# Optimization experiments

Hardware: AMD Instinct MI355X
Metric: run time of the kernel (lower is better)

## Reference

```python
import jax, jax.numpy as jnp
import numpy as np
from jax import lax

V, T, L = 32, 8192, 16
JITTER = 1e-6
LOG2PI = float(np.log(2.0 * np.pi))


def _state_space(lengthscale, variance):
    # Matern-3/2 SDE state space: lam = sqrt(3)/ell, P0 = diag(var, var*lam^2)
    lam = jnp.sqrt(3.0) / lengthscale                      # [L]
    z = jnp.zeros_like(lam)
    P0 = jnp.stack([jnp.stack([variance, z], -1),
                    jnp.stack([z, variance * lam ** 2], -1)], -2)  # [L,2,2]
    return lam, P0


def _state_transition(dt, lam):
    # dt: [v,T,1,1,1]; lam: [L] -> A = expm(F*dt): [v,L,T,2,2]
    lam3 = lam[:, None, None]                              # [L,1,1]
    ldt = dt * lam3                                        # [v,T,L,1,1]
    e = jnp.exp(-ldt)
    a11 = e * (ldt + 1.0)
    a12 = e * jnp.broadcast_to(dt, ldt.shape)
    a21 = -e * lam3 * ldt
    a22 = e * (1.0 - ldt)
    A = jnp.concatenate([jnp.concatenate([a11, a12], -1),
                         jnp.concatenate([a21, a22], -1)], -2)  # [v,T,L,2,2]
    return jnp.swapaxes(A, 1, 2)                           # [v,L,T,2,2]


def _mT(x):
    return jnp.swapaxes(x, -1, -2)


def _update_posterior(dt_nonzero, pseudo_y, pseudo_var, lengthscale, variance):
    v, Tn, Ln = pseudo_y.shape
    dtype = pseudo_y.dtype
    lam, P0 = _state_space(lengthscale, variance)
    P0b4 = P0[:, None]                                     # [L,1,2,2]
    zeros = jnp.zeros((v, 1, 1, 1, 1), dtype)

    # ---------------- filter (dt starts with 0) ----------------
    dt_f = jnp.concatenate([zeros, dt_nonzero], axis=1)    # [v,T,1,1,1]
    A_f = _state_transition(dt_f, lam)                     # [v,L,T,2,2]
    Q_f = P0b4 - A_f @ P0b4 @ _mT(A_f)
    A_t = jnp.moveaxis(A_f, 2, 0)                          # [T,v,L,2,2]
    Q_t = jnp.moveaxis(Q_f, 2, 0)
    ys = jnp.transpose(pseudo_y, (1, 0, 2))                # [T,v,L]
    rs = jnp.transpose(pseudo_var, (1, 0, 2))
    H = jnp.array([[1.0, 0.0]], dtype=dtype)               # [1,2]

    m0 = jnp.zeros((v, Ln, 2, 1), dtype)
    P0c = jnp.broadcast_to(P0, (v, Ln, 2, 2))

    def filt_step(carry, x):
        m, P = carry
        A, Q, y, r = x                                     # A/Q: [v,L,2,2]; y/r: [v,L]
        m_p = A @ m                                        # [v,L,2,1]
        P_p = A @ P @ _mT(A) + Q                           # [v,L,2,2]
        hat = (H @ m_p)[..., 0, 0]                         # [v,L]
        HP = H @ P_p                                       # [v,L,1,2]
        s = (HP @ H.T)[..., 0, 0] + r                      # [v,L] innovation var (1x1)
        d = y - hat                                        # [v,L]
        log_p = -0.5 * (d * d / s + jnp.log(s) + LOG2PI)   # MVN(1-dim) log prob
        W = _mT(HP) / (s + JITTER)[..., None, None]        # [v,L,2,1] Kalman gain
        m_new = m_p + W * d[..., None, None]
        P_new = P_p - W @ HP
        return (m_new, P_new), (m_new, P_new, log_p)

    (_, _), (m_fs_t, P_fs_t, log_ps) = lax.scan(filt_step, (m0, P0c), (A_t, Q_t, ys, rs))
    sum_log_p = jnp.sum(log_ps, axis=(0, 2))               # sum over T then L -> [v]
    m_fs = jnp.moveaxis(m_fs_t, 0, 2)                      # [v,L,T,2,1]
    P_fs = jnp.moveaxis(P_fs_t, 0, 2)                      # [v,L,T,2,2]

    # ---------------- RTS smoother (dt ends with 0) ----------------
    dt_s = jnp.concatenate([dt_nonzero, zeros], axis=1)
    A_s = _state_transition(dt_s, lam)
    Q_s = P0b4 - A_s @ P0b4 @ _mT(A_s)
    xs = (m_fs_t, P_fs_t, jnp.moveaxis(A_s, 2, 0), jnp.moveaxis(Q_s, 2, 0))
    I2 = jnp.eye(2, dtype=dtype)

    def smooth_step(carry, x):
        m_s, P_s = carry
        m_f, P_f, A, Q = x
        m_p = A @ m_f
        A_Pf = A @ P_f
        P_p = A_Pf @ _mT(A) + Q
        G = _mT(jnp.linalg.solve(P_p + JITTER * I2, A_Pf))  # [v,L,2,2]
        m_s2 = m_f + G @ (m_s - m_p)
        P_s2 = P_f - G @ (P_s - P_p) @ _mT(G)
        mZ = (H @ m_s2)[..., 0, 0]                          # [v,L]
        PZ = (H @ P_s2 @ H.T)[..., 0, 0]                    # [v,L]
        return (m_s2, P_s2), (mZ, PZ)

    carry0 = (m_fs[:, :, -1], P_fs[:, :, -1])
    (_, _), (mZ_t, PZ_t) = lax.scan(smooth_step, carry0, xs, reverse=True)
    m_ss_Z = jnp.transpose(mZ_t, (1, 2, 0))                 # [v,L,T]
    P_ss_Z = jnp.transpose(PZ_t, (1, 2, 0))                 # [v,L,T]
    return m_fs, P_fs, m_ss_Z, P_ss_Z, sum_log_p


def setup_inputs() -> dict:
    key = jax.random.key(0)
    k1, k2, k3, k4, k5 = jax.random.split(key, 5)
    dt_nonzero = jax.random.uniform(k1, (V, T - 1, 1, 1, 1), jnp.float32) * 0.05 + 0.01
    pseudo_y = jax.random.normal(k2, (V, T, L), jnp.float32)
    pseudo_var = jax.random.uniform(k3, (V, T, L), jnp.float32) * 0.5 + 0.1
    lengthscale = jax.random.uniform(k4, (L,), jnp.float32) + 1.0
    variance = jax.random.uniform(k5, (L,), jnp.float32) * 0.5 + 0.5
    return {"dt_nonzero": dt_nonzero, "pseudo_y": pseudo_y, "pseudo_var": pseudo_var,
            "lengthscale": lengthscale, "variance": variance}


def reference(dt_nonzero, pseudo_y, pseudo_var, lengthscale, variance):
    return _update_posterior(dt_nonzero, pseudo_y, pseudo_var, lengthscale, variance)
```

## Files before the change

### kernel.cpp

```cpp
#include <hip/hip_runtime.h>

#define TV 32
#define TT 8192
#define TL 16
#define NCHAIN (TV * TL)
#define CHUNK 32
#define WARM 96
#define NCHUNK (TT / CHUNK)
#define JIT 1e-6f
#define C_LOG2PI 1.837877066409345483560659472811f

#define BF 16

__global__ void __launch_bounds__(256)
__attribute__((amdgpu_waves_per_eu(2, 2)))
kf_fwd(
    const float* __restrict__ dt,
    const float* __restrict__ y,
    const float* __restrict__ rvar,
    const float* __restrict__ ls,
    const float* __restrict__ var,
    float* __restrict__ m_fs,
    float* __restrict__ P_fs,
    float* __restrict__ slp)
{
    const int tid   = blockIdx.x * 256 + threadIdx.x;
    const int chain = tid & (NCHAIN - 1);
    const int chunk = tid / NCHAIN;
    const int v = chain >> 4;
    const int l = chain & 15;

    const float lam = 1.7320508075688772f / ls[l];
    const float v0  = var[l];
    const float v1  = v0 * lam * lam;

    const int s  = chunk * CHUNK;
    const int e  = s + CHUNK;
    const int u0 = (s >= WARM) ? (s - WARM) : 0;

    const float* dtv = dt + (size_t)v * (TT - 1);
    const float* yp  = y    + (size_t)v * TT * TL + l;
    const float* rp  = rvar + (size_t)v * TT * TL + l;
    float4* mo4 = (float4*)(m_fs + (size_t)chain * TT * 2);
    float4* Po  = (float4*)(P_fs + (size_t)chain * TT * 4);

    float m0 = 0.f, m1 = 0.f;
    float P00 = v0, P01 = 0.f, P11 = v1;
    float acc = 0.f;
    float bm0 = 0.f, bm1 = 0.f;

    float ya[BF], ra[BF], da[BF];
    float yb[BF], rb[BF], db[BF];

#define FLOAD(Y, R, D, tb) {                                                  \
    _Pragma("unroll")                                                         \
    for (int j = 0; j < BF; ++j) {                                            \
        const int tt_ = (tb) + j;                                             \
        Y[j] = yp[(size_t)tt_ * TL];                                          \
        R[j] = rp[(size_t)tt_ * TL];                                          \
        D[j] = dtv[(tt_ >= 1) ? (tt_ - 1) : 0];                               \
    }                                                                         \
}

#define FCOMP(Y, R, D, tb) {                                                  \
    _Pragma("unroll")                                                         \
    for (int j = 0; j < BF; ++j) {                                            \
        const int tt_ = (tb) + j;                                             \
        const float dtc = (tt_ == 0) ? 0.f : D[j];  \
        const float ldt = dtc * lam;                                          \
        const float ee  = __expf(-ldt);                                       \
        const float a11 = ee * (ldt + 1.f);                                   \
        const float a12 = ee * dtc;                                           \
        const float a21 = -ee * lam * ldt;                                    \
        const float a22 = ee * (1.f - ldt);                                   \
        const float q00 = v0 - (a11 * a11 * v0 + a12 * a12 * v1);             \
        const float q01 = -(a11 * a21 * v0 + a12 * a22 * v1);                 \
        const float q11 = v1 - (a21 * a21 * v0 + a22 * a22 * v1);             \
        const float mp0 = a11 * m0 + a12 * m1;                                \
        const float mp1 = a21 * m0 + a22 * m1;                                \
        const float ap00 = a11 * P00 + a12 * P01;                             \
        const float ap01 = a11 * P01 + a12 * P11;                             \
        const float ap10 = a21 * P00 + a22 * P01;                             \
        const float ap11 = a21 * P01 + a22 * P11;                             \
        const float pp00 = ap00 * a11 + ap01 * a12 + q00;                     \
        const float pp01 = ap00 * a21 + ap01 * a22 + q01;                     \
        const float pp11 = ap10 * a21 + ap11 * a22 + q11;                     \
        const float ssv  = pp00 + R[j];                                       \
        const float d    = Y[j] - mp0;                                        \
        const float sinv = __builtin_amdgcn_rcpf(ssv + JIT);                  \
        const float W0 = pp00 * sinv;                                         \
        const float W1 = pp01 * sinv;                                         \
        m0 = mp0 + W0 * d;                                                    \
        m1 = mp1 + W1 * d;                                                    \
        P00 = pp00 - W0 * pp00;                                               \
        P01 = pp01 - W0 * pp01;                                               \
        P11 = pp11 - W1 * pp01;                                               \
        if (tt_ >= s) {            \
            acc += -0.5f * (d * d * __builtin_amdgcn_rcpf(ssv)                \
                            + __logf(ssv) + C_LOG2PI);                        \
            if ((j & 1) == 0) { bm0 = m0; bm1 = m1; }            \
            else mo4[tt_ >> 1] = make_float4(bm0, bm1, m0, m1);               \
            Po[tt_] = make_float4(P00, P01, P01, P11);                        \
        }                                                                     \
    }                                                                         \
}

    FLOAD(ya, ra, da, u0);
    for (int t = u0; t < e; t += 2 * BF) {
        FLOAD(yb, rb, db, t + BF);
        FCOMP(ya, ra, da, t);
        if (t + 2 * BF < e) FLOAD(ya, ra, da, t + 2 * BF);
        FCOMP(yb, rb, db, t + BF);
    }

    for (int mask = 8; mask >= 1; mask >>= 1)
        acc += __shfl_xor(acc, mask, 16);
    if ((threadIdx.x & 15) == 0)
        atomicAdd(&slp[v], acc);
}

#define BB 8

__global__ void __launch_bounds__(256)
__attribute__((amdgpu_waves_per_eu(2, 2)))
kf_bwd(
    const float* __restrict__ dt,
    const float* __restrict__ ls,
    const float* __restrict__ var,
    const float* __restrict__ m_fs,
    const float* __restrict__ P_fs,
    float* __restrict__ mZ,
    float* __restrict__ PZ)
{
    const int tid   = blockIdx.x * 256 + threadIdx.x;
    const int chain = tid & (NCHAIN - 1);
    const int chunk = tid / NCHAIN;
    const int v = chain >> 4;
    const int l = chain & 15;

    const float lam = 1.7320508075688772f / ls[l];
    const float v0  = var[l];
    const float v1  = v0 * lam * lam;

    const int s = chunk * CHUNK;
    const int e = s + CHUNK;
    int t0 = e - 1 + WARM;
    if (t0 > TT - 1) t0 = TT - 1;

    const float* dtv = dt + (size_t)v * (TT - 1);
    const float2* mi  = (const float2*)(m_fs + (size_t)chain * TT * 2);
    const float4* mi4 = (const float4*)(m_fs + (size_t)chain * TT * 2);
    const float4* Pi  = (const float4*)(P_fs + (size_t)chain * TT * 4);
    float* mo = mZ + (size_t)chain * TT;
    float* Po = PZ + (size_t)chain * TT;

    float2 mf2 = mi[t0];
    float4 Pf4 = Pi[t0];
    float ms0 = mf2.x, ms1 = mf2.y;
    float Ps00 = Pf4.x, Ps01 = Pf4.y, Ps11 = Pf4.w;
    if (t0 < e) { mo[t0] = ms0; Po[t0] = Ps00; }

    auto step = [&](float dtc, float mf0, float mf1,
                    float Pf00, float Pf01, float Pf11) {
        const float ldt = dtc * lam;
        const float ee  = __expf(-ldt);
        const float a11 = ee * (ldt + 1.f);
        const float a12 = ee * dtc;
        const float a21 = -ee * lam * ldt;
        const float a22 = ee * (1.f - ldt);
        const float q00 = v0 - (a11 * a11 * v0 + a12 * a12 * v1);
        const float q01 = -(a11 * a21 * v0 + a12 * a22 * v1);
        const float q11 = v1 - (a21 * a21 * v0 + a22 * a22 * v1);

        const float mp0 = a11 * mf0 + a12 * mf1;
        const float mp1 = a21 * mf0 + a22 * mf1;
        const float ap00 = a11 * Pf00 + a12 * Pf01;
        const float ap01 = a11 * Pf01 + a12 * Pf11;
        const float ap10 = a21 * Pf00 + a22 * Pf01;
        const float ap11 = a21 * Pf01 + a22 * Pf11;
        const float pp00 = ap00 * a11 + ap01 * a12 + q00;
        const float pp01 = ap00 * a21 + ap01 * a22 + q01;
        const float pp11 = ap10 * a21 + ap11 * a22 + q11;

        const float M00 = pp00 + JIT, M11 = pp11 + JIT;
        const float dinv = __builtin_amdgcn_rcpf(M00 * M11 - pp01 * pp01);
        const float G00 = (M11 * ap00 - pp01 * ap10) * dinv;
        const float G01 = (-pp01 * ap00 + M00 * ap10) * dinv;
        const float G10 = (M11 * ap01 - pp01 * ap11) * dinv;
        const float G11 = (-pp01 * ap01 + M00 * ap11) * dinv;

        const float dm0 = ms0 - mp0, dm1 = ms1 - mp1;
        const float nms0 = mf0 + G00 * dm0 + G01 * dm1;
        const float nms1 = mf1 + G10 * dm0 + G11 * dm1;
        const float D00 = Ps00 - pp00, D01 = Ps01 - pp01, D11 = Ps11 - pp11;
        const float gd00 = G00 * D00 + G01 * D01;
        const float gd01 = G00 * D01 + G01 * D11;
        const float gd10 = G10 * D00 + G11 * D01;
        const float gd11 = G10 * D01 + G11 * D11;
        ms0 = nms0; ms1 = nms1;
        Ps00 = Pf00 - (gd00 * G00 + gd01 * G01);
        Ps01 = Pf01 - (gd00 * G10 + gd01 * G11);
        Ps11 = Pf11 - (gd10 * G10 + gd11 * G11);
    };

    int t = t0 - 1;
    for (; t >= s && (t & 7) != 7; --t) {
        mf2 = mi[t]; Pf4 = Pi[t];
        step(dtv[t], mf2.x, mf2.y, Pf4.x, Pf4.y, Pf4.w);
        if (t < e) { mo[t] = ms0; Po[t] = Ps00; }
    }

    float b0m = 0.f, b1m = 0.f, b2m = 0.f, b3m = 0.f;
    float b0P = 0.f, b1P = 0.f, b2P = 0.f, b3P = 0.f;

    float4 Ma[BB / 2], Pa[BB]; float Da[BB];
    float4 Mb[BB / 2], Pb[BB]; float Db[BB];

#define BLOAD(M, P, D, tb) {                                                  \
    const int ib_ = ((tb) - 7) >> 1;                                          \
    _Pragma("unroll")                                                         \
    for (int j = 0; j < BB / 2; ++j) M[j] = mi4[ib_ + j];                     \
    _Pragma("unroll")                                                         \
    for (int j = 0; j < BB; ++j) {                                            \
        const int tt_ = (tb) - j;                                             \
        P[j] = Pi[tt_];                                                       \
        D[j] = dtv[tt_];                                                      \
    }                                                                         \
}

#define BCOMP(M, P, D, tb) {                                                  \
    const bool wr_ = (tb) < e;        \
    _Pragma("unroll")                                                         \
    for (int jj = 0; jj < BB; ++jj) {                                         \
        const int tt_ = (tb) - jj;                                            \
        const int k_  = 7 - jj;             \
        const float mf0_ = (k_ & 1) ? M[k_ >> 1].z : M[k_ >> 1].x;            \
        const float mf1_ = (k_ & 1) ? M[k_ >> 1].w : M[k_ >> 1].y;            \
        step(D[jj], mf0_, mf1_, P[jj].x, P[jj].y, P[jj].w);                   \
        const int slot_ = k_ & 3;               \
        if (slot_ == 3)      { b3m = ms0; b3P = Ps00; }                       \
        else if (slot_ == 2) { b2m = ms0; b2P = Ps00; }                       \
        else if (slot_ == 1) { b1m = ms0; b1P = Ps00; }                       \
        else {                                                                \
            b0m = ms0; b0P = Ps00;                                            \
            if (wr_) {                         \
                *(float4*)(mo + tt_) = make_float4(b0m, b1m, b2m, b3m);       \
                *(float4*)(Po + tt_) = make_float4(b0P, b1P, b2P, b3P);       \
            }                                                                 \
        }                                                                     \
    }                                                                         \
}

    int nb = (t - s + 1) >> 3;
    if (nb > 0) {
        BLOAD(Ma, Pa, Da, t);
        for (; nb >= 2; nb -= 2) {
            BLOAD(Mb, Pb, Db, t - BB);
            BCOMP(Ma, Pa, Da, t);
            t -= BB;
            if (nb > 2) BLOAD(Ma, Pa, Da, t - BB);
            BCOMP(Mb, Pb, Db, t);
            t -= BB;
        }
        if (nb == 1) BCOMP(Ma, Pa, Da, t);
    }
}

extern "C" void kernel_launch(void* const* d_in, const int* in_sizes, int n_in,
                              void* d_out, int out_size, void* d_ws, size_t ws_size,
                              hipStream_t stream) {
    const float* dt  = (const float*)d_in[0];
    const float* y   = (const float*)d_in[1];
    const float* rv  = (const float*)d_in[2];
    const float* ls  = (const float*)d_in[3];
    const float* var = (const float*)d_in[4];

    float* out  = (float*)d_out;
    float* m_fs = out;
    float* P_fs = m_fs + (size_t)NCHAIN * TT * 2;
    float* mZ   = P_fs + (size_t)NCHAIN * TT * 4;
    float* PZ   = mZ + (size_t)NCHAIN * TT;
    float* slp  = PZ + (size_t)NCHAIN * TT;

    hipMemsetAsync(slp, 0, TV * sizeof(float), stream);

    const int ntask = NCHAIN * NCHUNK;
    kf_fwd<<<ntask / 256, 256, 0, stream>>>(dt, y, rv, ls, var, m_fs, P_fs, slp);
    kf_bwd<<<ntask / 256, 256, 0, stream>>>(dt, ls, var, m_fs, P_fs, mZ, PZ);
}
```

Baseline: 330.0 us.

## Replace smoother warm-up with exact chunk affine-map composition and serial scan

The forward kernel now also composes, per chunk, the affine RTS smoother map (gain product, offset, covariance term) and writes it to workspace. A new small kernel scans these chunk maps backward across the sequence to give each chunk its exact starting smoothed state. The backward kernel then starts at the chunk end with no 96-step warm-up. This removes redundant warm-up work in the backward pass but adds per-step map composition in the forward pass and a serial scan kernel over 256 chunks with only 2 blocks. Scheduling barriers were also added around the prefetch loads.

```diff
diff --git a/kernel.cpp b/kernel.cpp
--- a/kernel.cpp
+++ b/kernel.cpp
@@ -9,8 +9,9 @@
 #define NCHUNK (TT / CHUNK)
 #define JIT 1e-6f
 #define C_LOG2PI 1.837877066409345483560659472811f
-
 #define BF 16
+#define BB 8
+#define SB 8
 
 __global__ void __launch_bounds__(256)
 __attribute__((amdgpu_waves_per_eu(2, 2)))
@@ -22,7 +23,10 @@
     const float* __restrict__ var,
     float* __restrict__ m_fs,
     float* __restrict__ P_fs,
-    float* __restrict__ slp)
+    float* __restrict__ slp,
+    float4* __restrict__ g4w,
+    float2* __restrict__ b2w,
+    float4* __restrict__ e4w)
 {
     const int tid   = blockIdx.x * 256 + threadIdx.x;
     const int chain = tid & (NCHAIN - 1);
@@ -48,6 +52,10 @@
     float P00 = v0, P01 = 0.f, P11 = v1;
     float acc = 0.f;
     float bm0 = 0.f, bm1 = 0.f;
+
+    float gam00 = 1.f, gam01 = 0.f, gam10 = 0.f, gam11 = 1.f;
+    float mbc0 = 0.f, mbc1 = 0.f;
+    float me00 = 0.f, me01 = 0.f, me11 = 0.f;
 
     float ya[BF], ra[BF], da[BF];
     float yb[BF], rb[BF], db[BF];
@@ -61,6 +69,41 @@
         D[j] = dtv[(tt_ >= 1) ? (tt_ - 1) : 0];                               \
     }                                                                         \
 }
+
+#define MAPCOMPOSE(SGNPLUS)                                                   \
+    {                                                                         \
+        const float M00_ = pp00 + JIT, M11_ = pp11 + JIT;                     \
+        const float dinv_ = __builtin_amdgcn_rcpf(M00_ * M11_ - pp01 * pp01); \
+        const float g00 = (M11_ * ap00 - pp01 * ap10) * dinv_;                \
+        const float g01 = (-pp01 * ap00 + M00_ * ap10) * dinv_;               \
+        const float g10 = (M11_ * ap01 - pp01 * ap11) * dinv_;                \
+        const float g11 = (-pp01 * ap01 + M00_ * ap11) * dinv_;               \
+        const float bb0 = m0 - (g00 * mp0 + g01 * mp1);                       \
+        const float bb1 = m1 - (g10 * mp0 + g11 * mp1);                       \
+        const float gp00 = g00 * pp00 + g01 * pp01;                           \
+        const float gp01 = g00 * pp01 + g01 * pp11;                           \
+        const float gp10 = g10 * pp00 + g11 * pp01;                           \
+        const float gp11 = g10 * pp01 + g11 * pp11;                           \
+        const float ee00 = P00 + (gp00 * g00 + gp01 * g01);                   \
+        const float ee01 = P01 + (gp00 * g10 + gp01 * g11);                   \
+        const float ee11 = P11 + (gp10 * g10 + gp11 * g11);                   \
+        mbc0 += gam00 * bb0 + gam01 * bb1;                                    \
+        mbc1 += gam10 * bb0 + gam11 * bb1;                                    \
+        const float u00 = gam00 * ee00 + gam01 * ee01;                        \
+        const float u01 = gam00 * ee01 + gam01 * ee11;                        \
+        const float u10 = gam10 * ee00 + gam11 * ee01;                        \
+        const float u11 = gam10 * ee01 + gam11 * ee11;                        \
+        const float r00 = u00 * gam00 + u01 * gam01;                          \
+        const float r01 = u00 * gam10 + u01 * gam11;                          \
+        const float r11 = u10 * gam10 + u11 * gam11;                          \
+        if (SGNPLUS) { me00 += r00; me01 += r01; me11 += r11; }               \
+        else         { me00 -= r00; me01 -= r01; me11 -= r11; }               \
+        const float ng00 = gam00 * g00 + gam01 * g10;                         \
+        const float ng01 = gam00 * g01 + gam01 * g11;                         \
+        const float ng10 = gam10 * g00 + gam11 * g10;                         \
+        const float ng11 = gam10 * g01 + gam11 * g11;                         \
+        gam00 = ng00; gam01 = ng01; gam10 = ng10; gam11 = ng11;               \
+    }
 
 #define FCOMP(Y, R, D, tb) {                                                  \
     _Pragma("unroll")                                                         \
@@ -85,6 +128,7 @@
         const float pp00 = ap00 * a11 + ap01 * a12 + q00;                     \
         const float pp01 = ap00 * a21 + ap01 * a22 + q01;                     \
         const float pp11 = ap10 * a21 + ap11 * a22 + q11;                     \
+        if (tt_ > s) MAPCOMPOSE((j & 1) != 0);            \
         const float ssv  = pp00 + R[j];                                       \
         const float d    = Y[j] - mp0;                                        \
         const float sinv = __builtin_amdgcn_rcpf(ssv + JIT);                  \
@@ -106,11 +150,45 @@
 }
 
     FLOAD(ya, ra, da, u0);
+    __builtin_amdgcn_sched_barrier(0);
     for (int t = u0; t < e; t += 2 * BF) {
         FLOAD(yb, rb, db, t + BF);
+        __builtin_amdgcn_sched_barrier(0);
         FCOMP(ya, ra, da, t);
-        if (t + 2 * BF < e) FLOAD(ya, ra, da, t + 2 * BF);
+        if (t + 2 * BF < e) {
+            FLOAD(ya, ra, da, t + 2 * BF);
+            __builtin_amdgcn_sched_barrier(0);
+        }
         FCOMP(yb, rb, db, t + BF);
+    }
+
+    if (chunk != NCHUNK - 1) {
+        const float dtc = dtv[e - 1];
+        const float ldt = dtc * lam;
+        const float ee  = __expf(-ldt);
+        const float a11 = ee * (ldt + 1.f);
+        const float a12 = ee * dtc;
+        const float a21 = -ee * lam * ldt;
+        const float a22 = ee * (1.f - ldt);
+        const float q00 = v0 - (a11 * a11 * v0 + a12 * a12 * v1);
+        const float q01 = -(a11 * a21 * v0 + a12 * a22 * v1);
+        const float q11 = v1 - (a21 * a21 * v0 + a22 * a22 * v1);
+        const float mp0 = a11 * m0 + a12 * m1;
+        const float mp1 = a21 * m0 + a22 * m1;
+        const float ap00 = a11 * P00 + a12 * P01;
+        const float ap01 = a11 * P01 + a12 * P11;
+        const float ap10 = a21 * P00 + a22 * P01;
+        const float ap11 = a21 * P01 + a22 * P11;
+        const float pp00 = ap00 * a11 + ap01 * a12 + q00;
+        const float pp01 = ap00 * a21 + ap01 * a22 + q01;
+        const float pp11 = ap10 * a21 + ap11 * a22 + q11;
+        MAPCOMPOSE(1);
+    }
+    {
+        const size_t mix = (size_t)chunk * NCHAIN + chain;
+        g4w[mix] = make_float4(gam00, gam01, gam10, gam11);
+        b2w[mix] = make_float2(mbc0, mbc1);
+        e4w[mix] = make_float4(me00, me01, me11, 0.f);
     }
 
     for (int mask = 8; mask >= 1; mask >>= 1)
@@ -119,7 +197,51 @@
         atomicAdd(&slp[v], acc);
 }
 
-#define BB 8
+__global__ void __launch_bounds__(256) kf_scan(
+    const float* __restrict__ m_fs,
+    const float* __restrict__ P_fs,
+    const float4* __restrict__ g4w,
+    const float2* __restrict__ b2w,
+    const float4* __restrict__ e4w,
+    float2* __restrict__ xmw,
+    float4* __restrict__ xPw)
+{
+    const int c = blockIdx.x * 256 + threadIdx.x;
+    const float* mt = m_fs + ((size_t)c * TT + (TT - 1)) * 2;
+    const float* Pt = P_fs + ((size_t)c * TT + (TT - 1)) * 4;
+    float xm0 = mt[0], xm1 = mt[1];
+    float XP00 = Pt[0], XP01 = Pt[1], XP11 = Pt[3];
+
+    float4 Gb[SB]; float2 Bb[SB]; float4 Eb[SB];
+    for (int kb = NCHUNK - 1; kb >= 0; kb -= SB) {
+#pragma unroll
+        for (int j = 0; j < SB; ++j) {
+            const size_t ix = (size_t)(kb - j) * NCHAIN + c;
+            Gb[j] = g4w[ix]; Bb[j] = b2w[ix]; Eb[j] = e4w[ix];
+        }
+        __builtin_amdgcn_sched_barrier(0);
+#pragma unroll
+        for (int j = 0; j < SB; ++j) {
+            const int k = kb - j;
+            const size_t ix = (size_t)k * NCHAIN + c;
+            xmw[ix] = make_float2(xm0, xm1);
+            xPw[ix] = make_float4(XP00, XP01, XP11, 0.f);
+            const float4 G = Gb[j]; const float2 B = Bb[j]; const float4 E = Eb[j];
+            const float nm0 = B.x + G.x * xm0 + G.y * xm1;
+            const float nm1 = B.y + G.z * xm0 + G.w * xm1;
+            const float u00 = G.x * XP00 + G.y * XP01;
+            const float u01 = G.x * XP01 + G.y * XP11;
+            const float u10 = G.z * XP00 + G.w * XP01;
+            const float u11 = G.z * XP01 + G.w * XP11;
+            const float r00 = u00 * G.x + u01 * G.y;
+            const float r01 = u00 * G.z + u01 * G.w;
+            const float r11 = u10 * G.z + u11 * G.w;
+            xm0 = nm0; xm1 = nm1;
+            if (k == NCHUNK - 1) { XP00 = E.x - r00; XP01 = E.y - r01; XP11 = E.z - r11; }
+            else                 { XP00 = E.x + r00; XP01 = E.y + r01; XP11 = E.z + r11; }
+        }
+    }
+}
 
 __global__ void __launch_bounds__(256)
 __attribute__((amdgpu_waves_per_eu(2, 2)))
@@ -129,12 +251,14 @@
     const float* __restrict__ var,
     const float* __restrict__ m_fs,
     const float* __restrict__ P_fs,
+    const float2* __restrict__ xmw,
+    const float4* __restrict__ xPw,
     float* __restrict__ mZ,
     float* __restrict__ PZ)
 {
     const int tid   = blockIdx.x * 256 + threadIdx.x;
     const int chain = tid & (NCHAIN - 1);
-    const int chunk = tid / NCHAIN;
+    const int k     = tid / NCHAIN;
     const int v = chain >> 4;
     const int l = chain & 15;
 
@@ -142,10 +266,8 @@
     const float v0  = var[l];
     const float v1  = v0 * lam * lam;
 
-    const int s = chunk * CHUNK;
+    const int s = k * CHUNK;
     const int e = s + CHUNK;
-    int t0 = e - 1 + WARM;
-    if (t0 > TT - 1) t0 = TT - 1;
 
     const float* dtv = dt + (size_t)v * (TT - 1);
     const float2* mi  = (const float2*)(m_fs + (size_t)chain * TT * 2);
@@ -154,11 +276,11 @@
     float* mo = mZ + (size_t)chain * TT;
     float* Po = PZ + (size_t)chain * TT;
 
-    float2 mf2 = mi[t0];
-    float4 Pf4 = Pi[t0];
-    float ms0 = mf2.x, ms1 = mf2.y;
-    float Ps00 = Pf4.x, Ps01 = Pf4.y, Ps11 = Pf4.w;
-    if (t0 < e) { mo[t0] = ms0; Po[t0] = Ps00; }
+    const size_t mix = (size_t)k * NCHAIN + chain;
+    const float2 x2 = xmw[mix];
+    const float4 xq = xPw[mix];
+    float ms0 = x2.x, ms1 = x2.y;
+    float Ps00 = xq.x, Ps01 = xq.y, Ps11 = xq.z;
 
     auto step = [&](float dtc, float mf0, float mf1,
                     float Pf00, float Pf01, float Pf11) {
@@ -203,11 +325,20 @@
         Ps11 = Pf11 - (gd10 * G10 + gd11 * G11);
     };
 
-    int t = t0 - 1;
+    int t;
+    if (k == NCHUNK - 1) {
+        mo[TT - 1] = ms0;
+        Po[TT - 1] = Ps00;
+        t = TT - 2;
+    } else {
+        t = e - 1;
+    }
+
     for (; t >= s && (t & 7) != 7; --t) {
-        mf2 = mi[t]; Pf4 = Pi[t];
+        const float2 mf2 = mi[t];
+        const float4 Pf4 = Pi[t];
         step(dtv[t], mf2.x, mf2.y, Pf4.x, Pf4.y, Pf4.w);
-        if (t < e) { mo[t] = ms0; Po[t] = Ps00; }
+        mo[t] = ms0; Po[t] = Ps00;
     }
 
     float b0m = 0.f, b1m = 0.f, b2m = 0.f, b3m = 0.f;
@@ -229,7 +360,6 @@
 }
 
 #define BCOMP(M, P, D, tb) {                                                  \
-    const bool wr_ = (tb) < e;        \
     _Pragma("unroll")                                                         \
     for (int jj = 0; jj < BB; ++jj) {                                         \
         const int tt_ = (tb) - jj;                                            \
@@ -243,7 +373,7 @@
         else if (slot_ == 1) { b1m = ms0; b1P = Ps00; }                       \
         else {                                                                \
             b0m = ms0; b0P = Ps00;                                            \
-            if (wr_) {                         \
+            {                                  \
                 *(float4*)(mo + tt_) = make_float4(b0m, b1m, b2m, b3m);       \
                 *(float4*)(Po + tt_) = make_float4(b0P, b1P, b2P, b3P);       \
             }                                                                 \
@@ -254,11 +384,16 @@
     int nb = (t - s + 1) >> 3;
     if (nb > 0) {
         BLOAD(Ma, Pa, Da, t);
+        __builtin_amdgcn_sched_barrier(0);
         for (; nb >= 2; nb -= 2) {
             BLOAD(Mb, Pb, Db, t - BB);
+            __builtin_amdgcn_sched_barrier(0);
             BCOMP(Ma, Pa, Da, t);
             t -= BB;
-            if (nb > 2) BLOAD(Ma, Pa, Da, t - BB);
+            if (nb > 2) {
+                BLOAD(Ma, Pa, Da, t - BB);
+                __builtin_amdgcn_sched_barrier(0);
+            }
             BCOMP(Mb, Pb, Db, t);
             t -= BB;
         }
@@ -282,9 +417,17 @@
     float* PZ   = mZ + (size_t)NCHAIN * TT;
     float* slp  = PZ + (size_t)NCHAIN * TT;
 
+    float4* g4w = (float4*)d_ws;
+    float4* e4w = g4w + (size_t)NCHUNK * NCHAIN;
+    float4* xPw = e4w + (size_t)NCHUNK * NCHAIN;
+    float2* b2w = (float2*)(xPw + (size_t)NCHUNK * NCHAIN);
+    float2* xmw = b2w + (size_t)NCHUNK * NCHAIN;
+
     hipMemsetAsync(slp, 0, TV * sizeof(float), stream);
 
     const int ntask = NCHAIN * NCHUNK;
-    kf_fwd<<<ntask / 256, 256, 0, stream>>>(dt, y, rv, ls, var, m_fs, P_fs, slp);
-    kf_bwd<<<ntask / 256, 256, 0, stream>>>(dt, ls, var, m_fs, P_fs, mZ, PZ);
-}
+    kf_fwd<<<ntask / 256, 256, 0, stream>>>(dt, y, rv, ls, var, m_fs, P_fs, slp,
+                                            g4w, b2w, e4w);
+    kf_scan<<<NCHAIN / 256, 256, 0, stream>>>(m_fs, P_fs, g4w, b2w, e4w, xmw, xPw);
+    kf_bwd<<<ntask / 256, 256, 0, stream>>>(dt, ls, var, m_fs, P_fs, xmw, xPw, mZ, PZ);
+}
```

Measured after the change: 308.7 us. 1.07x faster.
